# Kernel tuning notes

Hardware: AMD Instinct MI355X
Metric: run time of the kernel (lower is better)

The kernel has to match this reference:

```python
import jax, jax.numpy as jnp
import numpy as np

N = 100000   # nodes
E = 1600000  # edges
G = 512      # graphs in batch
IN_C, H1, H2, OUT_C = 3, 64, 128, 2


def setup_inputs() -> dict:
    key = jax.random.key(0)
    ks = jax.random.split(key, 9)
    x = jax.random.normal(ks[0], (N, IN_C), dtype=jnp.float32)
    edge_index = jax.random.randint(ks[1], (2, E), 0, N, dtype=jnp.int64)
    batch = jnp.sort(jax.random.randint(ks[2], (N,), 0, G, dtype=jnp.int64))
    # Glorot-ish init for weights, zeros for biases (as PyG GCNConv / nn.Linear defaults roughly)
    def glorot(k, shape):
        lim = float(np.sqrt(6.0 / (shape[0] + shape[1])))
        return jax.random.uniform(k, shape, jnp.float32, -lim, lim)
    W1 = glorot(ks[3], (IN_C, H1)); b1 = jnp.zeros((H1,), jnp.float32)
    W2 = glorot(ks[4], (H1, H2));   b2 = jnp.zeros((H2,), jnp.float32)
    Wfc = glorot(ks[5], (H2, OUT_C)); bfc = jnp.zeros((OUT_C,), jnp.float32)
    return {"x": x, "edge_index": edge_index, "batch": batch,
            "W1": W1, "b1": b1, "W2": W2, "b2": b2, "Wfc": Wfc, "bfc": bfc}


def _gcn_conv(x, W, b, src, dst, dinv):
    # PyG GCNConv: out = D^{-1/2} (A + I) D^{-1/2} X W + b
    xw = x @ W                                    # [N, F]
    norm = dinv[src] * dinv[dst]                  # per-edge symmetric norm
    agg = jax.ops.segment_sum(norm[:, None] * xw[src], dst, num_segments=x.shape[0])
    agg = agg + (dinv * dinv)[:, None] * xw       # self-loop contribution
    return agg + b


def reference(x, edge_index, batch, W1, b1, W2, b2, Wfc, bfc):
    src, dst = edge_index[0], edge_index[1]
    # degree with self-loops (edge weight 1), counted at edge targets as in PyG
    deg = jax.ops.segment_sum(jnp.ones((E,), x.dtype), dst, num_segments=N) + 1.0
    dinv = jax.lax.rsqrt(deg)
    h = jax.nn.relu(_gcn_conv(x, W1, b1, src, dst, dinv))
    h = jax.nn.relu(_gcn_conv(h, W2, b2, src, dst, dinv))
    # global_mean_pool over batch indices
    sums = jax.ops.segment_sum(h, batch, num_segments=G)          # [G, H2]
    cnt = jax.ops.segment_sum(jnp.ones((N,), h.dtype), batch, num_segments=G)
    pooled = sums / jnp.maximum(cnt, 1.0)[:, None]
    return pooled @ Wfc + bfc
```

## Files before the change

### kernel.cpp

```cpp
#include <hip/hip_runtime.h>

#define NN 100000
#define NE 1600000
#define NG 512
#define C_H1 64
#define C_H2 128
#define C_OUT 2

#define MM2_BLOCKS ((NN + 127) / 128)
#define NB ((NN + 255) >> 8)
#define PCHUNKS 512
#define PCHUNK_E (NE / PCHUNKS)
#define AT_S 68

__global__ void k_hist(const int* __restrict__ ei, int* __restrict__ hist) {
    __shared__ int lh[NB];
    int tid = threadIdx.x;
    int blk = blockIdx.x;
    for (int i = tid; i < NB; i += 256) lh[i] = 0;
    __syncthreads();
    int base = blk * PCHUNK_E;
    for (int e = base + tid; e < base + PCHUNK_E; e += 256)
        atomicAdd(&lh[ei[NE + e] >> 8], 1);
    __syncthreads();
    for (int i = tid; i < NB; i += 256) hist[i * PCHUNKS + blk] = lh[i];
}

__global__ void k_colscan0(const int* __restrict__ hist, int* __restrict__ offs,
                           int* __restrict__ btot) {
    __shared__ int sh[256];
    int b = blockIdx.x;
    int tid = threadIdx.x;
    int v0 = hist[b * PCHUNKS + 2 * tid];
    int v1 = hist[b * PCHUNKS + 2 * tid + 1];
    sh[tid] = v0 + v1;
    __syncthreads();
    for (int off = 1; off < 256; off <<= 1) {
        int v = (tid >= off) ? sh[tid - off] : 0;
        __syncthreads();
        sh[tid] += v;
        __syncthreads();
    }
    int base = (tid == 0) ? 0 : sh[tid - 1];
    offs[b * PCHUNKS + 2 * tid]     = base;
    offs[b * PCHUNKS + 2 * tid + 1] = base + v0;
    if (tid == 255) btot[b] = sh[255];
}

__global__ void k_bbase(const int* __restrict__ btot, int* __restrict__ bbase,
                        int* __restrict__ row_ptr) {
    __shared__ int sh[256];
    int tid = threadIdx.x;
    int v0 = (2 * tid     < NB) ? btot[2 * tid]     : 0;
    int v1 = (2 * tid + 1 < NB) ? btot[2 * tid + 1] : 0;
    sh[tid] = v0 + v1;
    __syncthreads();
    for (int off = 1; off < 256; off <<= 1) {
        int v = (tid >= off) ? sh[tid - off] : 0;
        __syncthreads();
        sh[tid] += v;
        __syncthreads();
    }
    int base = (tid == 0) ? 0 : sh[tid - 1];
    if (2 * tid     < NB) bbase[2 * tid]     = base;
    if (2 * tid + 1 < NB) bbase[2 * tid + 1] = base + v0;
    if (tid == 255) { bbase[NB] = sh[255]; row_ptr[NN] = sh[255]; }
}

__global__ void k_scatterA(const int* __restrict__ ei, const int* __restrict__ offs,
                           const int* __restrict__ bbase, int2* __restrict__ ed2) {
    __shared__ int lcur[NB];
    int tid = threadIdx.x;
    int blk = blockIdx.x;
    for (int i = tid; i < NB; i += 256) lcur[i] = bbase[i] + offs[i * PCHUNKS + blk];
    __syncthreads();
    int base = blk * PCHUNK_E;
    for (int e = base + tid; e < base + PCHUNK_E; e += 256) {
        int s = ei[e], d = ei[NE + e];
        int pos = atomicAdd(&lcur[d >> 8], 1);
        int2 v; v.x = s; v.y = d;
        ed2[pos] = v;
    }
}

__global__ void k_B1(const int2* __restrict__ ed2, const int* __restrict__ bbase,
                     float* __restrict__ dinv, int* __restrict__ row_ptr) {
    __shared__ int ldeg[256];
    __shared__ int sh[256];
    int b = blockIdx.x;
    int tid = threadIdx.x;
    int lo = b << 8;
    ldeg[tid] = 0;
    __syncthreads();
    int beg = bbase[b], end = bbase[b + 1];
    for (int j = beg + tid; j < end; j += 256)
        atomicAdd(&ldeg[ed2[j].y - lo], 1);
    __syncthreads();
    int d = ldeg[tid];
    int node = lo + tid;
    if (node < NN) dinv[node] = rsqrtf((float)d + 1.0f);
    sh[tid] = d;
    __syncthreads();
    for (int off = 1; off < 256; off <<= 1) {
        int v = (tid >= off) ? sh[tid - off] : 0;
        __syncthreads();
        sh[tid] += v;
        __syncthreads();
    }
    int excl = beg + ((tid == 0) ? 0 : sh[tid - 1]);
    if (node < NN) row_ptr[node] = excl;
}

__global__ void k_x4(const float* __restrict__ x, float4* __restrict__ x4) {
    int n = blockIdx.x * blockDim.x + threadIdx.x;
    if (n >= NN) return;
    float4 v; v.x = x[n * 3]; v.y = x[n * 3 + 1]; v.z = x[n * 3 + 2]; v.w = 0.f;
    x4[n] = v;
}

__global__ void k_scatterB(const int* __restrict__ row_ptr, const int2* __restrict__ ed2,
                           const float* __restrict__ dinv, const float4* __restrict__ x4,
                           int* __restrict__ ed, float4* __restrict__ aggx4) {
    __shared__ int   lcur[256];
    __shared__ float ldin[256];
    __shared__ float lax[256 * 3];
    int b = blockIdx.x;
    int lo = b << 8;
    int tid = threadIdx.x;
    int node = lo + tid;
    if (node <= NN) lcur[tid] = row_ptr[node < NN ? node : NN];
    else            lcur[tid] = 0;
    ldin[tid] = (node < NN) ? dinv[node] : 0.f;
    lax[tid] = 0.f; lax[256 + tid] = 0.f; lax[512 + tid] = 0.f;
    __syncthreads();
    int seg_beg = row_ptr[lo];
    int hi = lo + 256; if (hi > NN) hi = NN;
    int seg_end = row_ptr[hi];
    for (int j = seg_beg + tid; j < seg_end; j += 256) {
        int2 sd = ed2[j];
        int local = sd.y - lo;
        int pos = atomicAdd(&lcur[local], 1);
        float nrm = dinv[sd.x] * ldin[local];
        ed[pos] = sd.x;
        float4 xs = x4[sd.x];
        atomicAdd(&lax[local],       nrm * xs.x);
        atomicAdd(&lax[256 + local], nrm * xs.y);
        atomicAdd(&lax[512 + local], nrm * xs.z);
    }
    __syncthreads();
    if (node < NN) {
        float di = ldin[tid];
        float s2 = di * di;
        float4 xs = x4[node];
        float4 a;
        a.x = lax[tid]       + s2 * xs.x;
        a.y = lax[256 + tid] + s2 * xs.y;
        a.z = lax[512 + tid] + s2 * xs.z;
        a.w = di;
        aggx4[node] = a;
    }
}

__global__ void k_edge1(const int* __restrict__ row_ptr, const int* __restrict__ ed,
                        const float4* __restrict__ aggx4,
                        const float* __restrict__ W1, const float* __restrict__ b1,
                        float* __restrict__ agg1) {
    __shared__ float4 lp[256];
    int t = blockIdx.x * 256 + threadIdx.x;
    int n = t >> 6, c = t & 63;
    int lane = threadIdx.x & 63;
    int wbase = threadIdx.x & 192;

    float w0 = W1[c], w1 = W1[64 + c], w2 = W1[128 + c], bb = b1[c];
    float4 an = aggx4[n];
    float di = an.w;
    float hself = fmaxf(fmaf(an.x, w0, fmaf(an.y, w1, fmaf(an.z, w2, bb))), 0.f);
    float acc = di * di * hself;

    int beg = row_ptr[n], end = row_ptr[n + 1];
    for (int base = beg; base < end; base += 64) {
        int m = end - base; if (m > 64) m = 64;
        if (lane < m) {
            int s = ed[base + lane];
            float4 ax = aggx4[s];
            float4 p; p.x = ax.x; p.y = ax.y; p.z = ax.z; p.w = ax.w * di;
            lp[wbase + lane] = p;
        }
        int e = 0;
        for (; e + 3 < m; e += 4) {
            float4 p0 = lp[wbase + e];
            float4 p1 = lp[wbase + e + 1];
            float4 p2 = lp[wbase + e + 2];
            float4 p3 = lp[wbase + e + 3];
            float h0  = fmaxf(fmaf(p0.x, w0, fmaf(p0.y, w1, fmaf(p0.z, w2, bb))), 0.f);
            float h1v = fmaxf(fmaf(p1.x, w0, fmaf(p1.y, w1, fmaf(p1.z, w2, bb))), 0.f);
            float h2v = fmaxf(fmaf(p2.x, w0, fmaf(p2.y, w1, fmaf(p2.z, w2, bb))), 0.f);
            float h3v = fmaxf(fmaf(p3.x, w0, fmaf(p3.y, w1, fmaf(p3.z, w2, bb))), 0.f);
            acc = fmaf(p0.w, h0, acc);
            acc = fmaf(p1.w, h1v, acc);
            acc = fmaf(p2.w, h2v, acc);
            acc = fmaf(p3.w, h3v, acc);
        }
        for (; e < m; ++e) {
            float4 p = lp[wbase + e];
            float h = fmaxf(fmaf(p.x, w0, fmaf(p.y, w1, fmaf(p.z, w2, bb))), 0.f);
            acc = fmaf(p.w, h, acc);
        }
    }
    agg1[t] = acc;
}

__global__ __launch_bounds__(256)
void k_mm2pool(const float* __restrict__ agg1, const float* __restrict__ W2,
               const float* __restrict__ b2, const int* __restrict__ batch,
               float* __restrict__ pooled) {
    __shared__ float at[128 * AT_S];
    __shared__ float lpool[4 * C_H2];
    int tid = threadIdx.x;
    int bx  = blockIdx.x;

    const float4* a4 = (const float4*)(agg1 + (size_t)bx * 128 * C_H1);
    for (int i = tid; i < 128 * 16; i += 256) {
        int row = i >> 4, q = i & 15;
        *(float4*)&at[row * AT_S + q * 4] = a4[i];
    }
    for (int i = tid; i < 4 * C_H2; i += 256) lpool[i] = 0.f;
    __syncthreads();

    int tx = tid & 15;
    int my = tid >> 4;
    int c0 = tx * 4;

    float acc[8][8];
#pragma unroll
    for (int i = 0; i < 8; ++i)
#pragma unroll
        for (int j = 0; j < 8; ++j) acc[i][j] = 0.f;

#pragma unroll 1
    for (int k0 = 0; k0 < C_H1; k0 += 4) {
        float4 wfA[4], wfB[4];
#pragma unroll
        for (int kk = 0; kk < 4; ++kk) {
            wfA[kk] = *(const float4*)&W2[(k0 + kk) * C_H2 + c0];
            wfB[kk] = *(const float4*)&W2[(k0 + kk) * C_H2 + 64 + c0];
        }
#pragma unroll
        for (int i = 0; i < 8; ++i) {
            float4 af = *(const float4*)&at[(my + i * 16) * AT_S + k0];
#pragma unroll
            for (int kk = 0; kk < 4; ++kk) {
                float a = (kk == 0) ? af.x : (kk == 1) ? af.y : (kk == 2) ? af.z : af.w;
                acc[i][0] = fmaf(a, wfA[kk].x, acc[i][0]);
                acc[i][1] = fmaf(a, wfA[kk].y, acc[i][1]);
                acc[i][2] = fmaf(a, wfA[kk].z, acc[i][2]);
                acc[i][3] = fmaf(a, wfA[kk].w, acc[i][3]);
                acc[i][4] = fmaf(a, wfB[kk].x, acc[i][4]);
                acc[i][5] = fmaf(a, wfB[kk].y, acc[i][5]);
                acc[i][6] = fmaf(a, wfB[kk].z, acc[i][6]);
                acc[i][7] = fmaf(a, wfB[kk].w, acc[i][7]);
            }
        }
    }

    int nbase = bx * 128;
    int gbase = batch[nbase];
    int gidx[8];
#pragma unroll
    for (int i = 0; i < 8; ++i) {
        int node = nbase + my + i * 16;
        gidx[i] = (node < NN) ? batch[node] : -1;
    }

#pragma unroll
    for (int j = 0; j < 8; ++j) {
        int c = (j < 4) ? (c0 + j) : (64 + c0 + j - 4);
        float bb = b2[c];
        int run_g = -1;
        float rs = 0.f;
#pragma unroll
        for (int i = 0; i < 8; ++i) {
            if (gidx[i] < 0) break;
            float hcur = fmaxf(acc[i][j] + bb, 0.f);
            if (gidx[i] != run_g) {
                if (run_g >= 0) {
                    int slot = run_g - gbase;
                    if (slot < 4) atomicAdd(&lpool[slot * C_H2 + c], rs);
                    else          atomicAdd(&pooled[(run_g << 7) + c], rs);
                }
                run_g = gidx[i]; rs = hcur;
            } else {
                rs += hcur;
            }
        }
        if (run_g >= 0) {
            int slot = run_g - gbase;
            if (slot < 4) atomicAdd(&lpool[slot * C_H2 + c], rs);
            else          atomicAdd(&pooled[(run_g << 7) + c], rs);
        }
    }
    __syncthreads();
    for (int i = tid; i < 4 * C_H2; i += 256) {
        int slot = i >> 7, c = i & 127;
        int g = gbase + slot;
        float v = lpool[i];
        if (g < NG && v != 0.f) atomicAdd(&pooled[(g << 7) + c], v);
    }
}

__device__ __forceinline__ int lower_bound(const int* __restrict__ a, int n, int key) {
    int lo = 0, hi = n;
    while (lo < hi) { int mid = (lo + hi) >> 1; if (a[mid] < key) lo = mid + 1; else hi = mid; }
    return lo;
}

__global__ void k_fc(const float* __restrict__ pooled, const int* __restrict__ batch,
                     const float* __restrict__ Wfc, const float* __restrict__ bfc,
                     float* __restrict__ out) {
    int t = blockIdx.x * blockDim.x + threadIdx.x;
    if (t >= NG * C_OUT) return;
    int g = t >> 1, o = t & 1;
    int start = lower_bound(batch, NN, g);
    int end   = lower_bound(batch, NN, g + 1);
    float inv = 1.f / fmaxf((float)(end - start), 1.f);
    float s = bfc[o];
    for (int cc = 0; cc < C_H2; ++cc)
        s = fmaf(pooled[(g << 7) + cc] * inv, Wfc[cc * C_OUT + o], s);
    out[t] = s;
}

extern "C" void kernel_launch(void* const* d_in, const int* in_sizes, int n_in,
                              void* d_out, int out_size, void* d_ws, size_t ws_size,
                              hipStream_t stream) {
    const float* x     = (const float*)d_in[0];
    const int*   ei    = (const int*)d_in[1];
    const int*   batch = (const int*)d_in[2];
    const float* W1    = (const float*)d_in[3];
    const float* b1    = (const float*)d_in[4];
    const float* W2    = (const float*)d_in[5];
    const float* b2    = (const float*)d_in[6];
    const float* Wfc   = (const float*)d_in[7];
    const float* bfc   = (const float*)d_in[8];
    float* out = (float*)d_out;

    char* p = (char*)d_ws;
    auto alloc = [&](size_t bytes) { char* r = p; p += (bytes + 255) & ~size_t(255); return r; };
    float*  dinv    = (float*) alloc((size_t)NN * 4);
    int*    row_ptr = (int*)   alloc((size_t)(NN + 1) * 4);
    int*    btot    = (int*)   alloc((size_t)NB * 4);
    int*    bbase   = (int*)   alloc((size_t)(NB + 1) * 4);
    int*    hist    = (int*)   alloc((size_t)NB * PCHUNKS * 4);
    int*    offs    = (int*)   alloc((size_t)NB * PCHUNKS * 4);
    int2*   ed2     = (int2*)  alloc((size_t)NE * 8);
    int*    ed      = (int*)   alloc((size_t)NE * 4);
    float4* x4      = (float4*)alloc((size_t)NN * 16);
    float4* aggx4   = (float4*)alloc((size_t)NN * 16);
    float*  agg1    = (float*) alloc((size_t)(NN + 128) * C_H1 * 4);
    float*  pooled  = (float*) alloc((size_t)NG * C_H2 * 4);

    hipMemsetAsync(pooled, 0, (size_t)NG * C_H2 * 4, stream);
    k_hist    <<<PCHUNKS, 256, 0, stream>>>(ei, hist);
    k_colscan0<<<NB, 256, 0, stream>>>(hist, offs, btot);
    k_bbase   <<<1, 256, 0, stream>>>(btot, bbase, row_ptr);
    k_scatterA<<<PCHUNKS, 256, 0, stream>>>(ei, offs, bbase, ed2);
    k_B1      <<<NB, 256, 0, stream>>>(ed2, bbase, dinv, row_ptr);
    k_x4      <<<(NN + 255) / 256, 256, 0, stream>>>(x, x4);
    k_scatterB<<<NB, 256, 0, stream>>>(row_ptr, ed2, dinv, x4, ed, aggx4);
    k_edge1   <<<(NN * C_H1) / 256, 256, 0, stream>>>(row_ptr, ed, aggx4, W1, b1, agg1);
    k_mm2pool <<<MM2_BLOCKS, 256, 0, stream>>>(agg1, W2, b2, batch, pooled);
    k_fc      <<<(NG * C_OUT + 255) / 256, 256, 0, stream>>>(pooled, batch, Wfc, bfc, out);
}
```

Baseline: 233.1 us.

## Fuse layer-1 edge aggregation into the layer-2 matmul and pooling kernel

The per-node layer-1 gather/aggregate now runs inside the layer-2 matmul+pool kernel and writes each 128-node tile of layer-1 activations straight into shared memory. This removes the agg1 global buffer along with its write and read-back, and drops one kernel launch. The cost is parallelism: the edge phase now runs on about 782 blocks, each wave walking 32 nodes in sequence, instead of 25000 blocks. That may reduce latency hiding for the irregular neighbor gathers.

```diff
diff --git a/kernel.cpp b/kernel.cpp
--- a/kernel.cpp
+++ b/kernel.cpp
@@ -161,70 +161,69 @@
     }
 }
 
-__global__ void k_edge1(const int* __restrict__ row_ptr, const int* __restrict__ ed,
-                        const float4* __restrict__ aggx4,
-                        const float* __restrict__ W1, const float* __restrict__ b1,
-                        float* __restrict__ agg1) {
+__global__ __launch_bounds__(256)
+void k_edge_mm_pool(const int* __restrict__ row_ptr, const int* __restrict__ ed,
+                    const float4* __restrict__ aggx4,
+                    const float* __restrict__ W1, const float* __restrict__ b1,
+                    const float* __restrict__ W2, const float* __restrict__ b2,
+                    const int* __restrict__ batch, float* __restrict__ pooled) {
+    __shared__ float  at[128 * AT_S];
     __shared__ float4 lp[256];
-    int t = blockIdx.x * 256 + threadIdx.x;
-    int n = t >> 6, c = t & 63;
-    int lane = threadIdx.x & 63;
-    int wbase = threadIdx.x & 192;
-
-    float w0 = W1[c], w1 = W1[64 + c], w2 = W1[128 + c], bb = b1[c];
-    float4 an = aggx4[n];
-    float di = an.w;
-    float hself = fmaxf(fmaf(an.x, w0, fmaf(an.y, w1, fmaf(an.z, w2, bb))), 0.f);
-    float acc = di * di * hself;
-
-    int beg = row_ptr[n], end = row_ptr[n + 1];
-    for (int base = beg; base < end; base += 64) {
-        int m = end - base; if (m > 64) m = 64;
-        if (lane < m) {
-            int s = ed[base + lane];
-            float4 ax = aggx4[s];
-            float4 p; p.x = ax.x; p.y = ax.y; p.z = ax.z; p.w = ax.w * di;
-            lp[wbase + lane] = p;
-        }
-        int e = 0;
-        for (; e + 3 < m; e += 4) {
-            float4 p0 = lp[wbase + e];
-            float4 p1 = lp[wbase + e + 1];
-            float4 p2 = lp[wbase + e + 2];
-            float4 p3 = lp[wbase + e + 3];
-            float h0  = fmaxf(fmaf(p0.x, w0, fmaf(p0.y, w1, fmaf(p0.z, w2, bb))), 0.f);
-            float h1v = fmaxf(fmaf(p1.x, w0, fmaf(p1.y, w1, fmaf(p1.z, w2, bb))), 0.f);
-            float h2v = fmaxf(fmaf(p2.x, w0, fmaf(p2.y, w1, fmaf(p2.z, w2, bb))), 0.f);
-            float h3v = fmaxf(fmaf(p3.x, w0, fmaf(p3.y, w1, fmaf(p3.z, w2, bb))), 0.f);
-            acc = fmaf(p0.w, h0, acc);
-            acc = fmaf(p1.w, h1v, acc);
-            acc = fmaf(p2.w, h2v, acc);
-            acc = fmaf(p3.w, h3v, acc);
-        }
-        for (; e < m; ++e) {
-            float4 p = lp[wbase + e];
-            float h = fmaxf(fmaf(p.x, w0, fmaf(p.y, w1, fmaf(p.z, w2, bb))), 0.f);
-            acc = fmaf(p.w, h, acc);
-        }
-    }
-    agg1[t] = acc;
-}
-
-__global__ __launch_bounds__(256)
-void k_mm2pool(const float* __restrict__ agg1, const float* __restrict__ W2,
-               const float* __restrict__ b2, const int* __restrict__ batch,
-               float* __restrict__ pooled) {
-    __shared__ float at[128 * AT_S];
-    __shared__ float lpool[4 * C_H2];
-    int tid = threadIdx.x;
-    int bx  = blockIdx.x;
-
-    const float4* a4 = (const float4*)(agg1 + (size_t)bx * 128 * C_H1);
-    for (int i = tid; i < 128 * 16; i += 256) {
-        int row = i >> 4, q = i & 15;
-        *(float4*)&at[row * AT_S + q * 4] = a4[i];
-    }
+    __shared__ float  lpool[4 * C_H2];
+    int tid  = threadIdx.x;
+    int bx   = blockIdx.x;
+    int lane = tid & 63;
+    int w    = tid >> 6;
+    int wbase = w << 6;
+
     for (int i = tid; i < 4 * C_H2; i += 256) lpool[i] = 0.f;
+
+    {
+        int c = lane;
+        float w0 = W1[c], w1 = W1[64 + c], w2 = W1[128 + c], bb = b1[c];
+        int nodebase = bx * 128;
+        for (int r = w << 5; r < (w << 5) + 32; ++r) {
+            int n = nodebase + r;
+            float acc = 0.f;
+            if (n < NN) {
+                float4 an = aggx4[n];
+                float di = an.w;
+                float hself = fmaxf(fmaf(an.x, w0, fmaf(an.y, w1, fmaf(an.z, w2, bb))), 0.f);
+                acc = di * di * hself;
+                int beg = row_ptr[n], end = row_ptr[n + 1];
+                for (int base = beg; base < end; base += 64) {
+                    int m = end - base; if (m > 64) m = 64;
+                    if (lane < m) {
+                        int s = ed[base + lane];
+                        float4 ax = aggx4[s];
+                        float4 p; p.x = ax.x; p.y = ax.y; p.z = ax.z; p.w = ax.w * di;
+                        lp[wbase + lane] = p;
+                    }
+                    int e = 0;
+                    for (; e + 3 < m; e += 4) {
+                        float4 p0 = lp[wbase + e];
+                        float4 p1 = lp[wbase + e + 1];
+                        float4 p2 = lp[wbase + e + 2];
+                        float4 p3 = lp[wbase + e + 3];
+                        float h0  = fmaxf(fmaf(p0.x, w0, fmaf(p0.y, w1, fmaf(p0.z, w2, bb))), 0.f);
+                        float h1v = fmaxf(fmaf(p1.x, w0, fmaf(p1.y, w1, fmaf(p1.z, w2, bb))), 0.f);
+                        float h2v = fmaxf(fmaf(p2.x, w0, fmaf(p2.y, w1, fmaf(p2.z, w2, bb))), 0.f);
+                        float h3v = fmaxf(fmaf(p3.x, w0, fmaf(p3.y, w1, fmaf(p3.z, w2, bb))), 0.f);
+                        acc = fmaf(p0.w, h0, acc);
+                        acc = fmaf(p1.w, h1v, acc);
+                        acc = fmaf(p2.w, h2v, acc);
+                        acc = fmaf(p3.w, h3v, acc);
+                    }
+                    for (; e < m; ++e) {
+                        float4 p = lp[wbase + e];
+                        float h = fmaxf(fmaf(p.x, w0, fmaf(p.y, w1, fmaf(p.z, w2, bb))), 0.f);
+                        acc = fmaf(p.w, h, acc);
+                    }
+                }
+            }
+            at[r * AT_S + lane] = acc;
+        }
+    }
     __syncthreads();
 
     int tx = tid & 15;
@@ -355,18 +354,17 @@
     int*    ed      = (int*)   alloc((size_t)NE * 4);
     float4* x4      = (float4*)alloc((size_t)NN * 16);
     float4* aggx4   = (float4*)alloc((size_t)NN * 16);
-    float*  agg1    = (float*) alloc((size_t)(NN + 128) * C_H1 * 4);
     float*  pooled  = (float*) alloc((size_t)NG * C_H2 * 4);
 
     hipMemsetAsync(pooled, 0, (size_t)NG * C_H2 * 4, stream);
-    k_hist    <<<PCHUNKS, 256, 0, stream>>>(ei, hist);
-    k_colscan0<<<NB, 256, 0, stream>>>(hist, offs, btot);
-    k_bbase   <<<1, 256, 0, stream>>>(btot, bbase, row_ptr);
-    k_scatterA<<<PCHUNKS, 256, 0, stream>>>(ei, offs, bbase, ed2);
-    k_B1      <<<NB, 256, 0, stream>>>(ed2, bbase, dinv, row_ptr);
-    k_x4      <<<(NN + 255) / 256, 256, 0, stream>>>(x, x4);
-    k_scatterB<<<NB, 256, 0, stream>>>(row_ptr, ed2, dinv, x4, ed, aggx4);
-    k_edge1   <<<(NN * C_H1) / 256, 256, 0, stream>>>(row_ptr, ed, aggx4, W1, b1, agg1);
-    k_mm2pool <<<MM2_BLOCKS, 256, 0, stream>>>(agg1, W2, b2, batch, pooled);
-    k_fc      <<<(NG * C_OUT + 255) / 256, 256, 0, stream>>>(pooled, batch, Wfc, bfc, out);
-}
+    k_hist        <<<PCHUNKS, 256, 0, stream>>>(ei, hist);
+    k_colscan0    <<<NB, 256, 0, stream>>>(hist, offs, btot);
+    k_bbase       <<<1, 256, 0, stream>>>(btot, bbase, row_ptr);
+    k_scatterA    <<<PCHUNKS, 256, 0, stream>>>(ei, offs, bbase, ed2);
+    k_B1          <<<NB, 256, 0, stream>>>(ed2, bbase, dinv, row_ptr);
+    k_x4          <<<(NN + 255) / 256, 256, 0, stream>>>(x, x4);
+    k_scatterB    <<<NB, 256, 0, stream>>>(row_ptr, ed2, dinv, x4, ed, aggx4);
+    k_edge_mm_pool<<<MM2_BLOCKS, 256, 0, stream>>>(row_ptr, ed, aggx4, W1, b1, W2, b2,
+                                                   batch, pooled);
+    k_fc          <<<(NG * C_OUT + 255) / 256, 256, 0, stream>>>(pooled, batch, Wfc, bfc, out);
+}
```

Result: slower. 238.8 us (+2.4%).
